# Kernel optimization log

Hardware: AMD Instinct MI355X
Metric: run time of the kernel (lower is better)

## Reference

```python
import jax, jax.numpy as jnp
import numpy as np

EPS = 1e-7

def _masked_stats(x, w, k):
    # Parallel equivalent of the sequential Welford update_counter loop:
    # after the loop, mean = running mean, s = sum of squared deviations (M2),
    # std = sqrt(s / (k - 1)). Computed under no_grad in torch -> stop_gradient.
    m = jnp.sum(x * w, axis=0) / k
    s = jnp.sum(w * (x - m) ** 2, axis=0)
    std = jnp.sqrt(s / (k - 1.0))
    return jax.lax.stop_gradient(m), jax.lax.stop_gradient(std)

def _mlp(x, W1, b1, W2, b2):
    # MlpClass(d, d, 2*d, n_hidden=1) with relu act: d -> 2d -> d
    return jax.nn.relu(x @ W1 + b1) @ W2 + b2

def setup_inputs() -> dict:
    key = jax.random.key(0)
    ks = jax.random.split(key, 8)
    B, S, XD, DD = 8, 2048, 1024, 4096
    scale = 0.02
    return {
        "u": jax.random.normal(ks[0], (B, S, XD), jnp.float32),
        "v": jax.random.normal(ks[1], (B, S, DD), jnp.float32),
        "u_W1": jax.random.normal(ks[2], (XD, 2 * XD), jnp.float32) * scale,
        "u_b1": jnp.zeros((2 * XD,), jnp.float32),
        "u_W2": jax.random.normal(ks[3], (2 * XD, XD), jnp.float32) * scale,
        "u_b2": jnp.zeros((XD,), jnp.float32),
        "v_W1": jax.random.normal(ks[4], (DD, 2 * DD), jnp.float32) * scale,
        "v_b1": jnp.zeros((2 * DD,), jnp.float32),
        "v_W2": jax.random.normal(ks[5], (2 * DD, DD), jnp.float32) * scale,
        "v_b2": jnp.zeros((DD,), jnp.float32),
    }

def reference(u, v, u_W1, u_b1, u_W2, u_b2, v_W1, v_b1, v_W2, v_b2):
    u_ = u.reshape(-1, u.shape[-1]).astype(jnp.float32)  # [N, x_dim]
    v_ = v.reshape(-1, v.shape[-1]).astype(jnp.float32)  # [N, delta_dim]
    # nonzero-row mask; torch drops masked rows, we zero them (equivalent math,
    # static shapes). With randn inputs no row is masked.
    nz = jnp.any(u_ != 0, axis=-1) & jnp.any(v_ != 0, axis=-1)
    w = nz.astype(u_.dtype)[:, None]  # [N, 1]
    k = jnp.sum(w)
    u_mean, u_std = _masked_stats(u_, w, k)
    v_mean, v_std = _masked_stats(v_, w, k)
    u_input = (u_ - u_mean) / (u_std + EPS)
    v_input = (v_ - v_mean) / (v_std + EPS)
    out1 = _mlp(u_input, u_W1, u_b1, u_W2, u_b2) * w
    out2 = _mlp(v_input, v_W1, v_b1, v_W2, v_b2) * w
    return out1, out2
```

## Files before the change

kernel.cpp:

```cpp
#include <hip/hip_runtime.h>
#include <hip/hip_bf16.h>

#define NROWS 16384
#define XD 1024
#define DD 4096

typedef __attribute__((ext_vector_type(8))) short short8;
typedef __attribute__((ext_vector_type(4))) float f32x4;

__device__ __forceinline__ unsigned short f2bf(float f) {
  unsigned int u = __builtin_bit_cast(unsigned int, f);
  u += 0x7fffu + ((u >> 16) & 1u);
  return (unsigned short)(u >> 16);
}

__device__ __forceinline__ void load_lds16(const void* g, void* l) {
  __builtin_amdgcn_global_load_lds((const __attribute__((address_space(1))) void*)g,
                                   (__attribute__((address_space(3))) void*)l, 16, 0, 0);
}

__global__ __launch_bounds__(256) void mask_kernel(const float* __restrict__ u,
                                                   const float* __restrict__ v,
                                                   float* __restrict__ w) {
  int r = blockIdx.x;
  int t = threadIdx.x;
  const f32x4* up = (const f32x4*)(u + (size_t)r * XD);
  const f32x4* vp = (const f32x4*)(v + (size_t)r * DD);
  f32x4 a = up[t];
  int fu = __syncthreads_or((a.x != 0.f) | (a.y != 0.f) | (a.z != 0.f) | (a.w != 0.f));
  int fv = 0;
#pragma unroll
  for (int it = 0; it < DD / (256 * 4); ++it) {
    if (!fv) {
      f32x4 b = vp[it * 256 + t];
      fv = __syncthreads_or((b.x != 0.f) | (b.y != 0.f) | (b.z != 0.f) | (b.w != 0.f));
    }
  }
  if (t == 0) w[r] = (fu && fv) ? 1.f : 0.f;
}

__global__ __launch_bounds__(256) void ksum_kernel(const float* __restrict__ w,
                                                   float* __restrict__ kout) {
  __shared__ float sm[256];
  float s = 0.f;
  for (int i = threadIdx.x; i < NROWS; i += 256) s += w[i];
  sm[threadIdx.x] = s;
  __syncthreads();
  for (int st = 128; st > 0; st >>= 1) {
    if (threadIdx.x < st) sm[threadIdx.x] += sm[threadIdx.x + st];
    __syncthreads();
  }
  if (threadIdx.x == 0) kout[0] = sm[0];
}

__global__ __launch_bounds__(256) void colstats_partial(const float* __restrict__ X, int cols,
                                                        const float* __restrict__ w,
                                                        float* __restrict__ p1,
                                                        float* __restrict__ p2) {
  int c = blockIdx.x * 256 + threadIdx.x;
  int r0 = blockIdx.y * (NROWS / 64);
  float s1 = 0.f, s2 = 0.f;
  for (int r = r0; r < r0 + NROWS / 64; ++r) {
    float wr = w[r];
    float x = X[(size_t)r * cols + c];
    float xw = x * wr;
    s1 += xw;
    s2 += xw * x;
  }
  p1[(size_t)blockIdx.y * cols + c] = s1;
  p2[(size_t)blockIdx.y * cols + c] = s2;
}

__global__ __launch_bounds__(256) void colstats_final(const float* __restrict__ p1,
                                                      const float* __restrict__ p2,
                                                      const float* __restrict__ kptr, int cols,
                                                      float* __restrict__ mean,
                                                      float* __restrict__ inv) {
  int c = blockIdx.x * 256 + threadIdx.x;
  float s1 = 0.f, s2 = 0.f;
  for (int j = 0; j < 64; ++j) {
    s1 += p1[(size_t)j * cols + c];
    s2 += p2[(size_t)j * cols + c];
  }
  float k = kptr[0];
  float m = s1 / k;
  float s = s2 - s1 * s1 / k;
  float sd = sqrtf(fmaxf(s, 0.f) / (k - 1.f));
  mean[c] = m;
  inv[c] = 1.f / (sd + 1e-7f);
}

__global__ __launch_bounds__(256) void wt_kernel(const float* __restrict__ W, int R, int C,
                                                 unsigned short* __restrict__ T) {
  __shared__ unsigned short tile[64][65];
  int r0 = blockIdx.x * 64, c0 = blockIdx.y * 64;
  int tr = threadIdx.x >> 2;
  int tc = (threadIdx.x & 3) * 16;
  const float* src = W + (size_t)(r0 + tr) * C + c0 + tc;
#pragma unroll
  for (int i = 0; i < 16; i += 4) {
    f32x4 v4 = *(const f32x4*)(src + i);
    tile[tr][tc + i + 0] = f2bf(v4.x);
    tile[tr][tc + i + 1] = f2bf(v4.y);
    tile[tr][tc + i + 2] = f2bf(v4.z);
    tile[tr][tc + i + 3] = f2bf(v4.w);
  }
  __syncthreads();
  unsigned short* dst = T + (size_t)(c0 + tr) * R + r0 + tc;
  short8 o0, o1;
#pragma unroll
  for (int i = 0; i < 8; ++i) o0[i] = (short)tile[tc + i][tr];
#pragma unroll
  for (int i = 0; i < 8; ++i) o1[i] = (short)tile[tc + 8 + i][tr];
  *(short8*)(dst) = o0;
  *(short8*)(dst + 8) = o1;
}

__global__ __launch_bounds__(256) void norm_kernel(const float* __restrict__ X,
                                                   const float* __restrict__ mean,
                                                   const float* __restrict__ inv,
                                                   unsigned short* __restrict__ O,
                                                   int colmask, size_t n8) {
  size_t stride = (size_t)gridDim.x * 256;
  for (size_t i = (size_t)blockIdx.x * 256 + threadIdx.x; i < n8; i += stride) {
    int c8 = (int)(i & (size_t)colmask);
    const float* xp = X + i * 8;
    f32x4 a = *(const f32x4*)xp;
    f32x4 b = *(const f32x4*)(xp + 4);
    f32x4 m0 = *(const f32x4*)(mean + c8 * 8);
    f32x4 m1 = *(const f32x4*)(mean + c8 * 8 + 4);
    f32x4 i0 = *(const f32x4*)(inv + c8 * 8);
    f32x4 i1 = *(const f32x4*)(inv + c8 * 8 + 4);
    short8 p;
    p[0] = (short)f2bf((a.x - m0.x) * i0.x);
    p[1] = (short)f2bf((a.y - m0.y) * i0.y);
    p[2] = (short)f2bf((a.z - m0.z) * i0.z);
    p[3] = (short)f2bf((a.w - m0.w) * i0.w);
    p[4] = (short)f2bf((b.x - m1.x) * i1.x);
    p[5] = (short)f2bf((b.y - m1.y) * i1.y);
    p[6] = (short)f2bf((b.z - m1.z) * i1.z);
    p[7] = (short)f2bf((b.w - m1.w) * i1.w);
    *(short8*)(O + i * 8) = p;
  }
}

template <int EPI>
__global__ __launch_bounds__(512, 2) void gemm8p(const unsigned short* __restrict__ A,
                                                 const unsigned short* __restrict__ Bt,
                                                 const float* __restrict__ bias,
                                                 const float* __restrict__ wrow,
                                                 void* __restrict__ OutP,
                                                 int N, int K) {
  __shared__ char lds[131072];
  const int tid = threadIdx.x;
  const int lane = tid & 63;
  const int wave = tid >> 6;
  const int wr = wave >> 2;
  const int wc = wave & 3;

  const int gn = N >> 8;
  const int nwg = gridDim.x;
  const int gm = nwg / gn;
  const int bid = blockIdx.x;
  const int sw = (nwg & 7) ? bid : ((bid & 7) * (nwg >> 3) + (bid >> 3));
  const int SW_W = (gn >= 8) ? 8 : gn;
  const int SW_H = 32 / SW_W;
  int mt, nt;
  if ((gn % SW_W) == 0 && (gm % SW_H) == 0) {
    const int stn = gn / SW_W;
    const int st = sw >> 5;
    const int wi = sw & 31;
    mt = (st / stn) * SW_H + wi / SW_W;
    nt = (st % stn) * SW_W + wi % SW_W;
  } else {
    mt = sw / gn;
    nt = sw % gn;
  }
  const int m0 = mt << 8;
  const int n0 = nt << 8;

  const int srow = lane >> 3;
  const int scol = ((lane & 7) ^ srow) << 3;

  const int NT = K >> 6;
  f32x4 acc[8][4] = {};

  char* const Abase = lds + wr * 16384;
  char* const Bbase = lds + 65536 + (wc >> 1) * 16384;
  const int bcol = (wc & 1) * 64;
  const int fr = lane & 15;
  const int kbyte = (lane >> 4) << 4;

#define STAGE(T, BUF)                                                              \
  {                                                                                \
    const int k0_ = (T) << 6;                                                      \
    _Pragma("unroll") for (int i = 0; i < 4; ++i) {                                \
      const int row_ = i * 64 + wave * 8 + srow;                                   \
      const int co_ = (i * 8 + wave) * 1024;                                       \
      load_lds16(A + (size_t)(m0 + row_) * K + k0_ + scol, lds + (BUF)*32768 + co_); \
      load_lds16(Bt + (size_t)(n0 + row_) * K + k0_ + scol,                        \
                 lds + 65536 + (BUF)*32768 + co_);                                 \
    }                                                                              \
  }

  STAGE(0, 0);
  __syncthreads();

  for (int t = 0; t < NT; ++t) {
    const int buf = t & 1;
    const int ab = buf * 32768;
    if (t + 1 < NT) STAGE(t + 1, buf ^ 1);

    short8 bfr[2][4];
#pragma unroll
    for (int s = 0; s < 2; ++s)
#pragma unroll
      for (int g = 0; g < 4; ++g) {
        const int r = bcol + g * 16 + fr;
        const int kb = s * 64 + kbyte;
        bfr[s][g] = *(const short8*)(Bbase + ab + r * 128 + (kb ^ ((r & 7) << 4)));
      }

    short8 afA[2][2], afB[2][2];
#pragma unroll
    for (int p = 0; p < 2; ++p)
#pragma unroll
      for (int s = 0; s < 2; ++s) {
        const int r = p * 16 + fr;
        const int kb = s * 64 + kbyte;
        afA[p][s] = *(const short8*)(Abase + ab + r * 128 + (kb ^ ((r & 7) << 4)));
      }
#pragma unroll
    for (int q = 0; q < 4; ++q) {
      if (q < 3) {
#pragma unroll
        for (int p = 0; p < 2; ++p)
#pragma unroll
          for (int s = 0; s < 2; ++s) {
            const int r = ((q + 1) * 2 + p) * 16 + fr;
            const int kb = s * 64 + kbyte;
            short8 vf = *(const short8*)(Abase + ab + r * 128 + (kb ^ ((r & 7) << 4)));
            if (q & 1) afA[p][s] = vf; else afB[p][s] = vf;
          }
      }
      __builtin_amdgcn_s_setprio(1);
#pragma unroll
      for (int p = 0; p < 2; ++p)
#pragma unroll
        for (int s = 0; s < 2; ++s)
#pragma unroll
          for (int g = 0; g < 4; ++g) {
            const short8 av = (q & 1) ? afB[p][s] : afA[p][s];
            acc[q * 2 + p][g] =
                __builtin_amdgcn_mfma_f32_16x16x32_bf16(av, bfr[s][g], acc[q * 2 + p][g], 0, 0, 0);
          }
      __builtin_amdgcn_s_setprio(0);
    }
    __syncthreads();
  }

  const int colloc = wc * 64 + fr;
  const int rowb = wr * 128 + ((lane >> 4) << 2);
  if (EPI == 0) {
    unsigned short* H = (unsigned short*)OutP;
#pragma unroll
    for (int f = 0; f < 8; ++f)
#pragma unroll
      for (int g = 0; g < 4; ++g) {
        const int c = n0 + colloc + g * 16;
        const float b = bias[c];
#pragma unroll
        for (int r = 0; r < 4; ++r) {
          const int row = m0 + rowb + f * 16 + r;
          H[(size_t)row * N + c] = f2bf(fmaxf(acc[f][g][r] + b, 0.f));
        }
      }
  } else {
    float* O = (float*)OutP;
#pragma unroll
    for (int f = 0; f < 8; ++f)
#pragma unroll
      for (int g = 0; g < 4; ++g) {
        const int c = n0 + colloc + g * 16;
        const float b = bias[c];
#pragma unroll
        for (int r = 0; r < 4; ++r) {
          const int row = m0 + rowb + f * 16 + r;
          O[(size_t)row * N + c] = (acc[f][g][r] + b) * wrow[row];
        }
      }
  }
#undef STAGE
}

extern "C" void kernel_launch(void* const* d_in, const int* in_sizes, int n_in,
                              void* d_out, int out_size, void* d_ws, size_t ws_size,
                              hipStream_t stream) {
  const float* u    = (const float*)d_in[0];
  const float* v    = (const float*)d_in[1];
  const float* u_W1 = (const float*)d_in[2];
  const float* u_b1 = (const float*)d_in[3];
  const float* u_W2 = (const float*)d_in[4];
  const float* u_b2 = (const float*)d_in[5];
  const float* v_W1 = (const float*)d_in[6];
  const float* v_b1 = (const float*)d_in[7];
  const float* v_W2 = (const float*)d_in[8];
  const float* v_b2 = (const float*)d_in[9];
  float* out1 = (float*)d_out;
  float* out2 = out1 + (size_t)NROWS * XD;

  float* wsf = (float*)d_ws;
  size_t off = 0;
  float* w_     = wsf + off; off += NROWS;
  float* kv     = wsf + off; off += 16;
  float* u_mean = wsf + off; off += XD;
  float* u_inv  = wsf + off; off += XD;
  float* v_mean = wsf + off; off += DD;
  float* v_inv  = wsf + off; off += DD;
  float* p1u    = wsf + off; off += 64 * XD;
  float* p2u    = wsf + off; off += 64 * XD;
  float* p1v    = wsf + off; off += 64 * DD;
  float* p2v    = wsf + off; off += 64 * DD;

  size_t boff = (off * 4 + 255) & ~(size_t)255;
  unsigned short* W1Tu = (unsigned short*)((char*)d_ws + boff); boff += (size_t)(2 * XD) * XD * 2;
  unsigned short* W2Tu = (unsigned short*)((char*)d_ws + boff); boff += (size_t)XD * (2 * XD) * 2;
  unsigned short* W1Tv = (unsigned short*)((char*)d_ws + boff); boff += (size_t)(2 * DD) * DD * 2;
  unsigned short* W2Tv = (unsigned short*)((char*)d_ws + boff); boff += (size_t)DD * (2 * DD) * 2;
  size_t fixedB = (boff + 255) & ~(size_t)255;

  static const int chs[7] = {16384, 8192, 4096, 2048, 1024, 512, 256};
  int CHu = 256, CHv = 256;
  double best = 1e30;
  for (int a = 0; a < 7; ++a)
    for (int b = 0; b < 7; ++b) {
      int cu = chs[a], cv = chs[b];
      size_t need = fixedB + (size_t)cu * XD * 6 + (size_t)cv * DD * 6 + 1024;
      if (need > ws_size) continue;
      auto util = [](int nwg) { return nwg >= 256 ? 1.0 : nwg / 256.0; };
      double cost = 68.75 / util((cu >> 8) * 8) + 68.75 / util((cu >> 8) * 4) +
                    550.0 / util((cv >> 8) * 32) + 550.0 / util((cv >> 8) * 16);
      if (cost < best) { best = cost; CHu = cu; CHv = cv; }
    }

  size_t p = fixedB;
  unsigned short* unc  = (unsigned short*)((char*)d_ws + p); p += (size_t)CHu * XD * 2;
  unsigned short* uhid = (unsigned short*)((char*)d_ws + p); p += (size_t)CHu * (2 * XD) * 2;
  unsigned short* vnc  = (unsigned short*)((char*)d_ws + p); p += (size_t)CHv * DD * 2;
  unsigned short* vhid = (unsigned short*)((char*)d_ws + p);

  mask_kernel<<<NROWS, 256, 0, stream>>>(u, v, w_);
  ksum_kernel<<<1, 256, 0, stream>>>(w_, kv);
  colstats_partial<<<dim3(XD / 256, 64), 256, 0, stream>>>(u, XD, w_, p1u, p2u);
  colstats_partial<<<dim3(DD / 256, 64), 256, 0, stream>>>(v, DD, w_, p1v, p2v);
  colstats_final<<<XD / 256, 256, 0, stream>>>(p1u, p2u, kv, XD, u_mean, u_inv);
  colstats_final<<<DD / 256, 256, 0, stream>>>(p1v, p2v, kv, DD, v_mean, v_inv);

  wt_kernel<<<dim3(XD / 64, (2 * XD) / 64), 256, 0, stream>>>(u_W1, XD, 2 * XD, W1Tu);
  wt_kernel<<<dim3((2 * XD) / 64, XD / 64), 256, 0, stream>>>(u_W2, 2 * XD, XD, W2Tu);
  wt_kernel<<<dim3(DD / 64, (2 * DD) / 64), 256, 0, stream>>>(v_W1, DD, 2 * DD, W1Tv);
  wt_kernel<<<dim3((2 * DD) / 64, DD / 64), 256, 0, stream>>>(v_W2, 2 * DD, DD, W2Tv);

  for (int r0 = 0; r0 < NROWS; r0 += CHu) {
    size_t n8 = (size_t)CHu * XD / 8;
    int ng = (int)(n8 / 256 < 2048 ? n8 / 256 : 2048);
    norm_kernel<<<ng, 256, 0, stream>>>(u + (size_t)r0 * XD, u_mean, u_inv, unc, XD / 8 - 1, n8);
    gemm8p<0><<<(CHu >> 8) * ((2 * XD) >> 8), 512, 0, stream>>>(unc, W1Tu, u_b1, nullptr, uhid,
                                                                2 * XD, XD);
    gemm8p<1><<<(CHu >> 8) * (XD >> 8), 512, 0, stream>>>(uhid, W2Tu, u_b2, w_ + r0,
                                                          out1 + (size_t)r0 * XD, XD, 2 * XD);
  }
  for (int r0 = 0; r0 < NROWS; r0 += CHv) {
    size_t n8 = (size_t)CHv * DD / 8;
    int ng = (int)(n8 / 256 < 2048 ? n8 / 256 : 2048);
    norm_kernel<<<ng, 256, 0, stream>>>(v + (size_t)r0 * DD, v_mean, v_inv, vnc, DD / 8 - 1, n8);
    gemm8p<0><<<(CHv >> 8) * ((2 * DD) >> 8), 512, 0, stream>>>(vnc, W1Tv, v_b1, nullptr, vhid,
                                                                2 * DD, DD);
    gemm8p<1><<<(CHv >> 8) * (DD >> 8), 512, 0, stream>>>(vhid, W2Tv, v_b2, w_ + r0,
                                                          out2 + (size_t)r0 * DD, DD, 2 * DD);
  }
}
```

Before: 2.301 ms.

## Interleave global-to-LDS prefetch with MFMA phases using fine-grained waits and barriers

Restructures the bf16 GEMM main loop into four phases, each loading an A fragment slice from LDS, issuing a quarter of the next tile's global-to-LDS loads, and running MFMAs under raised priority. Explicit vmcnt/lgkmcnt waits and s_barrier calls replace the single end-of-iteration __syncthreads, so the next tile's loads no longer land all at once. The aim is to hide load latency and smooth memory traffic across the compute. The risk is more barriers per iteration and fragile hand-counted waits.

```diff
diff --git a/kernel.cpp b/kernel.cpp
--- a/kernel.cpp
+++ b/kernel.cpp
@@ -181,83 +181,142 @@
 
   const int srow = lane >> 3;
   const int scol = ((lane & 7) ^ srow) << 3;
+  const int fr = lane & 15;
+  const int kbyte = (lane >> 4) << 4;
 
   const int NT = K >> 6;
   f32x4 acc[8][4] = {};
 
-  char* const Abase = lds + wr * 16384;
-  char* const Bbase = lds + 65536 + (wc >> 1) * 16384;
-  const int bcol = (wc & 1) * 64;
-  const int fr = lane & 15;
-  const int kbyte = (lane >> 4) << 4;
-
-#define STAGE(T, BUF)                                                              \
-  {                                                                                \
-    const int k0_ = (T) << 6;                                                      \
-    _Pragma("unroll") for (int i = 0; i < 4; ++i) {                                \
-      const int row_ = i * 64 + wave * 8 + srow;                                   \
-      const int co_ = (i * 8 + wave) * 1024;                                       \
-      load_lds16(A + (size_t)(m0 + row_) * K + k0_ + scol, lds + (BUF)*32768 + co_); \
-      load_lds16(Bt + (size_t)(n0 + row_) * K + k0_ + scol,                        \
-                 lds + 65536 + (BUF)*32768 + co_);                                 \
-    }                                                                              \
-  }
-
-  STAGE(0, 0);
-  __syncthreads();
-
+#define STG_B(R0, NB, KN)                                                     \
+  load_lds16(Bt + (size_t)(n0 + (R0) + wave * 8 + srow) * K + (KN) + scol,    \
+             lds + 65536 + (NB)*32768 + (R0)*128 + wave * 1024)
+#define STG_A(R0, NB, KN)                                                     \
+  load_lds16(A + (size_t)(m0 + (R0) + wave * 8 + srow) * K + (KN) + scol,     \
+             lds + (NB)*32768 + (R0)*128 + wave * 1024)
+
+  STG_B(0, 0, 0); STG_B(64, 0, 0);
+  STG_B(128, 0, 0); STG_B(192, 0, 0);
+  STG_A(0, 0, 0); STG_A(128, 0, 0);
+  STG_A(64, 0, 0); STG_A(192, 0, 0);
+  asm volatile("s_waitcnt vmcnt(2)" ::: "memory");
+  __builtin_amdgcn_sched_barrier(0);
+  __builtin_amdgcn_s_barrier();
+
+  short8 bfr[2][4], afr[2][2];
   for (int t = 0; t < NT; ++t) {
-    const int buf = t & 1;
-    const int ab = buf * 32768;
-    if (t + 1 < NT) STAGE(t + 1, buf ^ 1);
-
-    short8 bfr[2][4];
+    const int buf = t & 1, nb = buf ^ 1;
+    const int kn = (t + 1) << 6;
+    const char* Ab = lds + buf * 32768;
+    const char* Bb = lds + 65536 + buf * 32768;
+    const bool pf = (t + 1 < NT);
+
 #pragma unroll
     for (int s = 0; s < 2; ++s)
 #pragma unroll
       for (int g = 0; g < 4; ++g) {
-        const int r = bcol + g * 16 + fr;
-        const int kb = s * 64 + kbyte;
-        bfr[s][g] = *(const short8*)(Bbase + ab + r * 128 + (kb ^ ((r & 7) << 4)));
-      }
-
-    short8 afA[2][2], afB[2][2];
-#pragma unroll
-    for (int p = 0; p < 2; ++p)
+        const int r = wc * 64 + g * 16 + fr;
+        bfr[s][g] = *(const short8*)(Bb + r * 128 + ((s * 64 + kbyte) ^ ((r & 7) << 4)));
+      }
+#pragma unroll
+    for (int f = 0; f < 2; ++f)
 #pragma unroll
       for (int s = 0; s < 2; ++s) {
-        const int r = p * 16 + fr;
-        const int kb = s * 64 + kbyte;
-        afA[p][s] = *(const short8*)(Abase + ab + r * 128 + (kb ^ ((r & 7) << 4)));
-      }
-#pragma unroll
-    for (int q = 0; q < 4; ++q) {
-      if (q < 3) {
-#pragma unroll
-        for (int p = 0; p < 2; ++p)
-#pragma unroll
-          for (int s = 0; s < 2; ++s) {
-            const int r = ((q + 1) * 2 + p) * 16 + fr;
-            const int kb = s * 64 + kbyte;
-            short8 vf = *(const short8*)(Abase + ab + r * 128 + (kb ^ ((r & 7) << 4)));
-            if (q & 1) afA[p][s] = vf; else afB[p][s] = vf;
-          }
-      }
-      __builtin_amdgcn_s_setprio(1);
-#pragma unroll
-      for (int p = 0; p < 2; ++p)
-#pragma unroll
-        for (int s = 0; s < 2; ++s)
-#pragma unroll
-          for (int g = 0; g < 4; ++g) {
-            const short8 av = (q & 1) ? afB[p][s] : afA[p][s];
-            acc[q * 2 + p][g] =
-                __builtin_amdgcn_mfma_f32_16x16x32_bf16(av, bfr[s][g], acc[q * 2 + p][g], 0, 0, 0);
-          }
-      __builtin_amdgcn_s_setprio(0);
+        const int r = wr * 128 + f * 16 + fr;
+        afr[f][s] = *(const short8*)(Ab + r * 128 + ((s * 64 + kbyte) ^ ((r & 7) << 4)));
+      }
+    if (pf) { STG_B(0, nb, kn); STG_B(64, nb, kn); }
+    __builtin_amdgcn_s_barrier();
+    asm volatile("s_waitcnt lgkmcnt(0)" ::: "memory");
+    __builtin_amdgcn_sched_barrier(0);
+    __builtin_amdgcn_s_setprio(1);
+#pragma unroll
+    for (int f = 0; f < 2; ++f)
+#pragma unroll
+      for (int s = 0; s < 2; ++s)
+#pragma unroll
+        for (int g = 0; g < 4; ++g)
+          acc[f][g] = __builtin_amdgcn_mfma_f32_16x16x32_bf16(afr[f][s], bfr[s][g], acc[f][g], 0, 0, 0);
+    __builtin_amdgcn_s_setprio(0);
+    __builtin_amdgcn_s_barrier();
+
+#pragma unroll
+    for (int f = 0; f < 2; ++f)
+#pragma unroll
+      for (int s = 0; s < 2; ++s) {
+        const int r = wr * 128 + 32 + f * 16 + fr;
+        afr[f][s] = *(const short8*)(Ab + r * 128 + ((s * 64 + kbyte) ^ ((r & 7) << 4)));
+      }
+    if (pf) { STG_B(128, nb, kn); STG_B(192, nb, kn); }
+    __builtin_amdgcn_s_barrier();
+    asm volatile("s_waitcnt lgkmcnt(0)" ::: "memory");
+    __builtin_amdgcn_sched_barrier(0);
+    __builtin_amdgcn_s_setprio(1);
+#pragma unroll
+    for (int f = 0; f < 2; ++f)
+#pragma unroll
+      for (int s = 0; s < 2; ++s)
+#pragma unroll
+        for (int g = 0; g < 4; ++g)
+          acc[2 + f][g] = __builtin_amdgcn_mfma_f32_16x16x32_bf16(afr[f][s], bfr[s][g], acc[2 + f][g], 0, 0, 0);
+    __builtin_amdgcn_s_setprio(0);
+    if (pf) {
+      asm volatile("s_waitcnt vmcnt(4)" ::: "memory");
+    } else {
+      asm volatile("s_waitcnt vmcnt(0)" ::: "memory");
     }
-    __syncthreads();
-  }
+    __builtin_amdgcn_sched_barrier(0);
+    __builtin_amdgcn_s_barrier();
+
+#pragma unroll
+    for (int f = 0; f < 2; ++f)
+#pragma unroll
+      for (int s = 0; s < 2; ++s) {
+        const int r = wr * 128 + 64 + f * 16 + fr;
+        afr[f][s] = *(const short8*)(Ab + r * 128 + ((s * 64 + kbyte) ^ ((r & 7) << 4)));
+      }
+    if (pf) { STG_A(0, nb, kn); STG_A(128, nb, kn); }
+    __builtin_amdgcn_s_barrier();
+    asm volatile("s_waitcnt lgkmcnt(0)" ::: "memory");
+    __builtin_amdgcn_sched_barrier(0);
+    __builtin_amdgcn_s_setprio(1);
+#pragma unroll
+    for (int f = 0; f < 2; ++f)
+#pragma unroll
+      for (int s = 0; s < 2; ++s)
+#pragma unroll
+        for (int g = 0; g < 4; ++g)
+          acc[4 + f][g] = __builtin_amdgcn_mfma_f32_16x16x32_bf16(afr[f][s], bfr[s][g], acc[4 + f][g], 0, 0, 0);
+    __builtin_amdgcn_s_setprio(0);
+    __builtin_amdgcn_s_barrier();
+
+#pragma unroll
+    for (int f = 0; f < 2; ++f)
+#pragma unroll
+      for (int s = 0; s < 2; ++s) {
+        const int r = wr * 128 + 96 + f * 16 + fr;
+        afr[f][s] = *(const short8*)(Ab + r * 128 + ((s * 64 + kbyte) ^ ((r & 7) << 4)));
+      }
+    if (pf) { STG_A(64, nb, kn); STG_A(192, nb, kn); }
+    __builtin_amdgcn_s_barrier();
+    asm volatile("s_waitcnt lgkmcnt(0)" ::: "memory");
+    __builtin_amdgcn_sched_barrier(0);
+    __builtin_amdgcn_s_setprio(1);
+#pragma unroll
+    for (int f = 0; f < 2; ++f)
+#pragma unroll
+      for (int s = 0; s < 2; ++s)
+#pragma unroll
+        for (int g = 0; g < 4; ++g)
+          acc[6 + f][g] = __builtin_amdgcn_mfma_f32_16x16x32_bf16(afr[f][s], bfr[s][g], acc[6 + f][g], 0, 0, 0);
+    __builtin_amdgcn_s_setprio(0);
+    if (pf) {
+      asm volatile("s_waitcnt vmcnt(2)" ::: "memory");
+      __builtin_amdgcn_sched_barrier(0);
+    }
+    __builtin_amdgcn_s_barrier();
+  }
+#undef STG_A
+#undef STG_B
 
   const int colloc = wc * 64 + fr;
   const int rowb = wr * 128 + ((lane >> 4) << 2);
@@ -290,7 +349,6 @@
         }
       }
   }
-#undef STAGE
 }
 
 extern "C" void kernel_launch(void* const* d_in, const int* in_sizes, int n_in,
```

New measurement: 2.404 ms. +4.5%, slower.

## Split GEMM tile across 16 waves with 64x64 warp tiles

Applied to the files above, without the earlier changes.

Reorganizes the bf16 GEMM from 8 waves each computing a 128x64 sub-tile into 16 waves (1024 threads) each computing 64x64, with a simpler staging layout and no A-fragment double buffering. The aim is more waves per CU to hide LDS and MFMA latency. In exchange, each wave reads more LDS data per MFMA and register pressure is constrained by the larger block size.

```diff
diff --git a/kernel.cpp b/kernel.cpp
--- a/kernel.cpp
+++ b/kernel.cpp
@@ -145,18 +145,18 @@
 }
 
 template <int EPI>
-__global__ __launch_bounds__(512, 2) void gemm8p(const unsigned short* __restrict__ A,
-                                                 const unsigned short* __restrict__ Bt,
-                                                 const float* __restrict__ bias,
-                                                 const float* __restrict__ wrow,
-                                                 void* __restrict__ OutP,
-                                                 int N, int K) {
+__global__ __launch_bounds__(1024, 4) void gemm8p(const unsigned short* __restrict__ A,
+                                                  const unsigned short* __restrict__ Bt,
+                                                  const float* __restrict__ bias,
+                                                  const float* __restrict__ wrow,
+                                                  void* __restrict__ OutP,
+                                                  int N, int K) {
   __shared__ char lds[131072];
   const int tid = threadIdx.x;
   const int lane = tid & 63;
   const int wave = tid >> 6;
-  const int wr = wave >> 2;
-  const int wc = wave & 3;
+  const int wm = wave >> 2;
+  const int wn = wave & 3;
 
   const int gn = N >> 8;
   const int nwg = gridDim.x;
@@ -179,92 +179,67 @@
   const int m0 = mt << 8;
   const int n0 = nt << 8;
 
-  const int srow = lane >> 3;
-  const int scol = ((lane & 7) ^ srow) << 3;
+  const int srow = tid >> 3;
+  const int scol = (((tid & 7) ^ (srow & 7)) << 3);
 
   const int NT = K >> 6;
-  f32x4 acc[8][4] = {};
-
-  char* const Abase = lds + wr * 16384;
-  char* const Bbase = lds + 65536 + (wc >> 1) * 16384;
-  const int bcol = (wc & 1) * 64;
+  f32x4 acc[4][4] = {};
+
   const int fr = lane & 15;
   const int kbyte = (lane >> 4) << 4;
 
-#define STAGE(T, BUF)                                                              \
-  {                                                                                \
-    const int k0_ = (T) << 6;                                                      \
-    _Pragma("unroll") for (int i = 0; i < 4; ++i) {                                \
-      const int row_ = i * 64 + wave * 8 + srow;                                   \
-      const int co_ = (i * 8 + wave) * 1024;                                       \
-      load_lds16(A + (size_t)(m0 + row_) * K + k0_ + scol, lds + (BUF)*32768 + co_); \
-      load_lds16(Bt + (size_t)(n0 + row_) * K + k0_ + scol,                        \
-                 lds + 65536 + (BUF)*32768 + co_);                                 \
-    }                                                                              \
+#define STAGE(T, BUF)                                                                   \
+  {                                                                                     \
+    const int k0_ = (T) << 6;                                                           \
+    _Pragma("unroll") for (int i = 0; i < 2; ++i) {                                     \
+      const int row_ = srow + i * 128;                                                  \
+      load_lds16(A + (size_t)(m0 + row_) * K + k0_ + scol,                              \
+                 lds + (BUF)*65536 + i * 16384 + tid * 16);                             \
+      load_lds16(Bt + (size_t)(n0 + row_) * K + k0_ + scol,                             \
+                 lds + (BUF)*65536 + 32768 + i * 16384 + tid * 16);                     \
+    }                                                                                   \
   }
 
   STAGE(0, 0);
   __syncthreads();
 
+  short8 af[4], bf_[4];
   for (int t = 0; t < NT; ++t) {
     const int buf = t & 1;
-    const int ab = buf * 32768;
+    const char* Ab = lds + buf * 65536;
+    const char* Bb = lds + buf * 65536 + 32768;
     if (t + 1 < NT) STAGE(t + 1, buf ^ 1);
 
-    short8 bfr[2][4];
-#pragma unroll
-    for (int s = 0; s < 2; ++s)
+#pragma unroll
+    for (int s = 0; s < 2; ++s) {
+#pragma unroll
+      for (int f = 0; f < 4; ++f) {
+        const int r = wm * 64 + f * 16 + fr;
+        af[f] = *(const short8*)(Ab + r * 128 + ((s * 64 + kbyte) ^ ((r & 7) << 4)));
+      }
 #pragma unroll
       for (int g = 0; g < 4; ++g) {
-        const int r = bcol + g * 16 + fr;
-        const int kb = s * 64 + kbyte;
-        bfr[s][g] = *(const short8*)(Bbase + ab + r * 128 + (kb ^ ((r & 7) << 4)));
-      }
-
-    short8 afA[2][2], afB[2][2];
-#pragma unroll
-    for (int p = 0; p < 2; ++p)
-#pragma unroll
-      for (int s = 0; s < 2; ++s) {
-        const int r = p * 16 + fr;
-        const int kb = s * 64 + kbyte;
-        afA[p][s] = *(const short8*)(Abase + ab + r * 128 + (kb ^ ((r & 7) << 4)));
-      }
-#pragma unroll
-    for (int q = 0; q < 4; ++q) {
-      if (q < 3) {
-#pragma unroll
-        for (int p = 0; p < 2; ++p)
-#pragma unroll
-          for (int s = 0; s < 2; ++s) {
-            const int r = ((q + 1) * 2 + p) * 16 + fr;
-            const int kb = s * 64 + kbyte;
-            short8 vf = *(const short8*)(Abase + ab + r * 128 + (kb ^ ((r & 7) << 4)));
-            if (q & 1) afA[p][s] = vf; else afB[p][s] = vf;
-          }
+        const int r = wn * 64 + g * 16 + fr;
+        bf_[g] = *(const short8*)(Bb + r * 128 + ((s * 64 + kbyte) ^ ((r & 7) << 4)));
       }
       __builtin_amdgcn_s_setprio(1);
 #pragma unroll
-      for (int p = 0; p < 2; ++p)
-#pragma unroll
-        for (int s = 0; s < 2; ++s)
-#pragma unroll
-          for (int g = 0; g < 4; ++g) {
-            const short8 av = (q & 1) ? afB[p][s] : afA[p][s];
-            acc[q * 2 + p][g] =
-                __builtin_amdgcn_mfma_f32_16x16x32_bf16(av, bfr[s][g], acc[q * 2 + p][g], 0, 0, 0);
-          }
+      for (int f = 0; f < 4; ++f)
+#pragma unroll
+        for (int g = 0; g < 4; ++g)
+          acc[f][g] = __builtin_amdgcn_mfma_f32_16x16x32_bf16(af[f], bf_[g], acc[f][g], 0, 0, 0);
       __builtin_amdgcn_s_setprio(0);
     }
     __syncthreads();
   }
-
-  const int colloc = wc * 64 + fr;
-  const int rowb = wr * 128 + ((lane >> 4) << 2);
+#undef STAGE
+
+  const int colloc = wn * 64 + fr;
+  const int rowb = wm * 64 + ((lane >> 4) << 2);
   if (EPI == 0) {
     unsigned short* H = (unsigned short*)OutP;
 #pragma unroll
-    for (int f = 0; f < 8; ++f)
+    for (int f = 0; f < 4; ++f)
 #pragma unroll
       for (int g = 0; g < 4; ++g) {
         const int c = n0 + colloc + g * 16;
@@ -278,7 +253,7 @@
   } else {
     float* O = (float*)OutP;
 #pragma unroll
-    for (int f = 0; f < 8; ++f)
+    for (int f = 0; f < 4; ++f)
 #pragma unroll
       for (int g = 0; g < 4; ++g) {
         const int c = n0 + colloc + g * 16;
@@ -290,7 +265,6 @@
         }
       }
   }
-#undef STAGE
 }
 
 extern "C" void kernel_launch(void* const* d_in, const int* in_sizes, int n_in,
@@ -365,18 +339,18 @@
     size_t n8 = (size_t)CHu * XD / 8;
     int ng = (int)(n8 / 256 < 2048 ? n8 / 256 : 2048);
     norm_kernel<<<ng, 256, 0, stream>>>(u + (size_t)r0 * XD, u_mean, u_inv, unc, XD / 8 - 1, n8);
-    gemm8p<0><<<(CHu >> 8) * ((2 * XD) >> 8), 512, 0, stream>>>(unc, W1Tu, u_b1, nullptr, uhid,
-                                                                2 * XD, XD);
-    gemm8p<1><<<(CHu >> 8) * (XD >> 8), 512, 0, stream>>>(uhid, W2Tu, u_b2, w_ + r0,
-                                                          out1 + (size_t)r0 * XD, XD, 2 * XD);
+    gemm8p<0><<<(CHu >> 8) * ((2 * XD) >> 8), 1024, 0, stream>>>(unc, W1Tu, u_b1, nullptr, uhid,
+                                                                 2 * XD, XD);
+    gemm8p<1><<<(CHu >> 8) * (XD >> 8), 1024, 0, stream>>>(uhid, W2Tu, u_b2, w_ + r0,
+                                                           out1 + (size_t)r0 * XD, XD, 2 * XD);
   }
   for (int r0 = 0; r0 < NROWS; r0 += CHv) {
     size_t n8 = (size_t)CHv * DD / 8;
     int ng = (int)(n8 / 256 < 2048 ? n8 / 256 : 2048);
     norm_kernel<<<ng, 256, 0, stream>>>(v + (size_t)r0 * DD, v_mean, v_inv, vnc, DD / 8 - 1, n8);
-    gemm8p<0><<<(CHv >> 8) * ((2 * DD) >> 8), 512, 0, stream>>>(vnc, W1Tv, v_b1, nullptr, vhid,
-                                                                2 * DD, DD);
-    gemm8p<1><<<(CHv >> 8) * (DD >> 8), 512, 0, stream>>>(vhid, W2Tv, v_b2, w_ + r0,
-                                                          out2 + (size_t)r0 * DD, DD, 2 * DD);
-  }
-}
+    gemm8p<0><<<(CHv >> 8) * ((2 * DD) >> 8), 1024, 0, stream>>>(vnc, W1Tv, v_b1, nullptr, vhid,
+                                                                 2 * DD, DD);
+    gemm8p<1><<<(CHv >> 8) * (DD >> 8), 1024, 0, stream>>>(vhid, W2Tv, v_b2, w_ + r0,
+                                                           out2 + (size_t)r0 * DD, DD, 2 * DD);
+  }
+}
```

Result: no change. 2.271 ms (median of 2 runs) (-1.3%).
